# Optimization experiments

Hardware: AMD Instinct MI355X
Metric: run time of the kernel (lower is better)

Reference implementation:

```python
import jax, jax.numpy as jnp
import numpy as np
from jax import lax

BS, CNT, W, P, E, K, L = 32, 128, 2048, 1024, 8, 25, 2


def setup_inputs() -> dict:
    key = jax.random.key(0)
    ks = jax.random.split(key, 12)
    s = lambda k, shape, scale: jax.random.normal(k, shape, dtype=jnp.float32) * scale
    return {
        "x": s(ks[0], (BS, CNT, W), 1.0),
        "conv_w": s(ks[1], (L, E, 1, K), 0.2),
        "conv_b": s(ks[2], (L, E), 0.02),
        "wq": s(ks[3], (L, P, W), 0.02),
        "bq": s(ks[4], (L, P), 0.02),
        "wk": s(ks[5], (L, P, W), 0.02),
        "bk": s(ks[6], (L, P), 0.02),
        "wv": s(ks[7], (L, P, W), 0.02),
        "bv": s(ks[8], (L, P), 0.02),
        "wo": s(ks[9], (L, W, P), 0.02),
        "bo": s(ks[10], (L, W), 0.02),
    }


def _moe(x, w, b):
    # x: [bs, cnt, W]; w: [E, 1, K]; b: [E]
    bs, cnt, d = x.shape
    xf = x.reshape(bs * cnt, 1, d)
    pad = K // 2
    y = lax.conv_general_dilated(
        xf, w, window_strides=(1,), padding=[(pad, pad)],
        dimension_numbers=("NCH", "OIH", "NCH"))  # [bs*cnt, E, W]
    y = y + b[None, :, None]
    return y.mean(axis=1).reshape(bs, cnt, d)


def _fe(x, wq, bq, wk, bk, wv, bv, wo, bo):
    # x: [bs, cnt, W]; projections to P, FFT-domain attention, back to W
    q = jnp.einsum("bcw,pw->bcp", x, wq) + bq
    k = jnp.einsum("bcw,pw->bcp", x, wk) + bk
    v = jnp.einsum("bcw,pw->bcp", x, wv) + bv
    q_fft = jnp.fft.fft(q, axis=-1)
    k_fft = jnp.fft.fft(k, axis=-1)
    v_fft = jnp.fft.fft(v, axis=-1)
    scale = jnp.sqrt(jnp.float32(P))
    weighted = (k_fft * jnp.conj(q_fft)) / scale * v_fft
    wv_real = jnp.fft.ifft(weighted, axis=-1).real.astype(x.dtype)
    return jnp.einsum("bcp,wp->bcw", wv_real, wo) + bo


def reference(x, conv_w, conv_b, wq, bq, wk, bk, wv, bv, wo, bo):
    for l in range(L):
        x = _moe(x, conv_w[l], conv_b[l])
        x = _fe(x, wq[l], bq[l], wk[l], bk[l], wv[l], bv[l], wo[l], bo[l])
    return x
```

## Files before the change

### kernel.cpp

```cpp
#include <hip/hip_runtime.h>
#include <hip/hip_bf16.h>

#define BSZ 32
#define CNTS 128
#define WD 2048
#define PD 1024
#define ED 8
#define KSZ 25
#define LN 2
#define MROWS (BSZ*CNTS)
#define QKVN (3*PD)
#define NWL (PD*WD)

typedef _Float16 f16;
typedef __attribute__((ext_vector_type(8))) _Float16 f16x8;
typedef __attribute__((ext_vector_type(4))) float f32x4;
typedef __attribute__((ext_vector_type(2))) float f32x2;

#define PI_F 3.14159265358979323846f
#define PAD(a) ((a) + ((a) >> 5))

__global__ __launch_bounds__(256) void cvt_layer(
    const float* __restrict__ wq, const float* __restrict__ wk,
    const float* __restrict__ wv, const float* __restrict__ wo,
    f16* __restrict__ wqkv16, f16* __restrict__ wo16)
{
    const int i = (blockIdx.x * 256 + threadIdx.x) * 4;
    const float* src;
    f16* dst;
    if (i < 3*NWL) {
        dst = wqkv16 + i;
        src = (i < NWL) ? wq + i : (i < 2*NWL) ? wk + (i - NWL) : wv + (i - 2*NWL);
    } else {
        dst = wo16 + (i - 3*NWL);
        src = wo + (i - 3*NWL);
    }
    const float4 v = *(const float4*)src;
    f16 o[4];
    o[0] = (f16)v.x; o[1] = (f16)v.y; o[2] = (f16)v.z; o[3] = (f16)v.w;
    *(ushort4*)dst = *(const ushort4*)o;
}

template<typename IT>
__global__ __launch_bounds__(256) void conv_moe(
    const IT* __restrict__ xin,
    const float* __restrict__ cw,
    const float* __restrict__ cb,
    f16* __restrict__ xo)
{
    __shared__ float srow[WD];
    __shared__ float swb[KSZ];
    __shared__ float sbb;
    const int tid = threadIdx.x;
    const size_t row = blockIdx.x;
    if (tid < KSZ) {
        float s = 0.f;
        for (int e = 0; e < ED; ++e) s += cw[e*KSZ + tid];
        swb[tid] = s * (1.f/ED);
    }
    if (tid == 32) {
        float s = 0.f;
        for (int e = 0; e < ED; ++e) s += cb[e];
        sbb = s * (1.f/ED);
    }
    const IT* xr = xin + row*WD;
    for (int i = tid; i < WD; i += 256) srow[i] = (float)xr[i];
    __syncthreads();
    const float bb = sbb;
    for (int t0 = 0; t0 < WD; t0 += 256) {
        const int t = t0 + tid;
        float acc = bb;
        #pragma unroll
        for (int k = 0; k < KSZ; ++k) {
            const int idx = t + k - (KSZ/2);
            const float xv = (idx >= 0 && idx < WD) ? srow[idx] : 0.f;
            acc = fmaf(xv, swb[k], acc);
        }
        xo[row*WD + t] = (f16)acc;
    }
}

template<typename OT>
__global__ __launch_bounds__(256, 2) void gemm_f16(
    const f16* __restrict__ A,
    const f16* __restrict__ B,
    const float* __restrict__ c0, const float* __restrict__ c1, const float* __restrict__ c2,
    OT* __restrict__ out,
    const int K, const int N)
{
    __shared__ f16 sA[128*64];
    __shared__ f16 sB[128*64];
    const int tid  = threadIdx.x;
    const int m0   = blockIdx.x * 128;
    const int n0   = blockIdx.y * 128;
    const int lane = tid & 63;
    const int wave = tid >> 6;
    const int wm   = (wave >> 1) * 64;
    const int wn   = (wave & 1) * 64;
    const int quad = lane >> 4;
    const int r16  = lane & 15;

    f32x4 acc[4][4] = {};

    int arow[4], aoff[4];
    #pragma unroll
    for (int t = 0; t < 4; ++t) {
        const int s = tid + 256*t;
        const int row = s >> 3;
        const int sc8 = ((s & 7) ^ (row & 7)) * 8;
        arow[t] = row;
        aoff[t] = row * K + sc8;
    }

    int aBase[4], aXor[4], bBase[4], bXor[4];
    #pragma unroll
    for (int i = 0; i < 4; ++i) {
        const int ra = wm + i*16 + r16;
        aBase[i] = ra << 3; aXor[i] = ra & 7;
        const int rb = wn + i*16 + r16;
        bBase[i] = rb << 3; bXor[i] = rb & 7;
    }

    const size_t mK = (size_t)m0 * K;
    const size_t nK = (size_t)n0 * K;

    for (int kb = 0; kb < K; kb += 64) {
        #pragma unroll
        for (int t = 0; t < 4; ++t) {
            const int s = tid + 256*t;
            __builtin_amdgcn_global_load_lds(
                (const __attribute__((address_space(1))) unsigned int*)(A + mK + aoff[t] + kb),
                (__attribute__((address_space(3))) unsigned int*)&sA[s*8], 16, 0, 0);
            __builtin_amdgcn_global_load_lds(
                (const __attribute__((address_space(1))) unsigned int*)(B + nK + aoff[t] + kb),
                (__attribute__((address_space(3))) unsigned int*)&sB[s*8], 16, 0, 0);
        }
        __syncthreads();

        #pragma unroll
        for (int ks = 0; ks < 2; ++ks) {
            const int c = ks*4 + quad;
            f16x8 af[4], bfm[4];
            #pragma unroll
            for (int i = 0; i < 4; ++i)
                af[i] = *(const f16x8*)&sA[(aBase[i] | (c ^ aXor[i])) * 8];
            #pragma unroll
            for (int j = 0; j < 4; ++j)
                bfm[j] = *(const f16x8*)&sB[(bBase[j] | (c ^ bXor[j])) * 8];
            #pragma unroll
            for (int i = 0; i < 4; ++i)
                #pragma unroll
                for (int j = 0; j < 4; ++j)
                    acc[i][j] = __builtin_amdgcn_mfma_f32_16x16x32_f16(af[i], bfm[j], acc[i][j], 0, 0, 0);
        }
        __syncthreads();
    }

    #pragma unroll
    for (int j = 0; j < 4; ++j) {
        const int col = n0 + wn + j*16 + r16;
        const float bv = (col < 1024) ? c0[col] : (col < 2048) ? c1[col-1024] : c2[col-2048];
        #pragma unroll
        for (int i = 0; i < 4; ++i) {
            #pragma unroll
            for (int r = 0; r < 4; ++r) {
                const int rowg = m0 + wm + i*16 + quad*4 + r;
                out[(size_t)rowg*N + col] = (OT)(acc[i][j][r] + bv);
            }
        }
    }
}

__global__ __launch_bounds__(512, 2) void gemm256(
    const f16* __restrict__ A,
    const f16* __restrict__ B,
    const float* __restrict__ c0, const float* __restrict__ c1, const float* __restrict__ c2,
    f16* __restrict__ out,
    const int K, const int N)
{
    __shared__ __align__(16) f16 sA[2][2][128*64];
    __shared__ __align__(16) f16 sB[2][2][128*64];

    const int tid  = threadIdx.x;
    const int lane = tid & 63;
    const int wave = tid >> 6;
    const int wr   = wave >> 2;
    const int wc   = wave & 3;
    const int quad = lane >> 4;
    const int r16  = lane & 15;
    const int xr   = r16 & 7;
    const int bHalf = wc >> 1;
    const int bRowB = (wc & 1) * 64;

    const int nwg  = gridDim.x;
    const int orig = blockIdx.x;
    const int wgid = (orig & 7) * (nwg >> 3) + (orig >> 3);
    const int m0   = (wgid & 15) * 256;
    const int n0   = (wgid >> 4) * 256;

    f32x4 acc[8][4] = {};
    f16x8 bf[4][2];

    int soff[2];
    #pragma unroll
    for (int t = 0; t < 2; ++t) {
        const int s = tid + 512*t;
        const int row = s >> 3;
        soff[t] = row * K + (((s & 7) ^ (row & 7)) * 8);
    }

    const f16* Abase[2] = { A + (size_t)m0 * K, A + (size_t)(m0 + 128) * K };
    const f16* Bbase[2] = { B + (size_t)n0 * K, B + (size_t)(n0 + 128) * K };

    #define STAGE(DST, BUF, HALF, GBASE)                                          \
      { _Pragma("unroll") for (int t = 0; t < 2; ++t) {                           \
          __builtin_amdgcn_global_load_lds(                                       \
            (const __attribute__((address_space(1))) unsigned int*)((GBASE) + soff[t]), \
            (__attribute__((address_space(3))) unsigned int*)&DST[BUF][HALF][(tid + 512*t)*8], \
            16, 0, 0); } }

    #define LDFRAG(MAT, BUF, HALF, ROW, C) \
      (*(const f16x8*)&MAT[BUF][HALF][ (((ROW)*8) + ((C) ^ xr)) * 8 ])

    #define WAIT_NONE
    #define WAIT_P4  if (!klast) { asm volatile("s_waitcnt vmcnt(4)" ::: "memory"); } \
                     else        { asm volatile("s_waitcnt vmcnt(0)" ::: "memory"); }
    #define WAIT_P8  if (!klast) { asm volatile("s_waitcnt vmcnt(4)" ::: "memory"); }

    #define PHASE(BUF, Q, WAIT, ...)                                              \
    {                                                                             \
      if ((Q) == 0) {                                                             \
        _Pragma("unroll") for (int j = 0; j < 4; ++j) {                           \
          bf[j][0] = LDFRAG(sB, BUF, bHalf, bRowB + j*16 + r16, quad);            \
          bf[j][1] = LDFRAG(sB, BUF, bHalf, bRowB + j*16 + r16, 4 + quad);        \
        }                                                                         \
      }                                                                           \
      f16x8 a00 = LDFRAG(sA, BUF, wr, (2*(Q))*16   + r16, quad);                  \
      f16x8 a01 = LDFRAG(sA, BUF, wr, (2*(Q))*16   + r16, 4 + quad);              \
      f16x8 a10 = LDFRAG(sA, BUF, wr, (2*(Q)+1)*16 + r16, quad);                  \
      f16x8 a11 = LDFRAG(sA, BUF, wr, (2*(Q)+1)*16 + r16, 4 + quad);              \
      __VA_ARGS__;                                                                \
      __builtin_amdgcn_s_barrier();                                               \
      asm volatile("s_waitcnt lgkmcnt(0)" ::: "memory");                          \
      __builtin_amdgcn_sched_barrier(0);                                          \
      __builtin_amdgcn_s_setprio(1);                                              \
      _Pragma("unroll") for (int j = 0; j < 4; ++j) {                             \
        acc[2*(Q)][j]   = __builtin_amdgcn_mfma_f32_16x16x32_f16(a00, bf[j][0], acc[2*(Q)][j],   0,0,0); \
        acc[2*(Q)+1][j] = __builtin_amdgcn_mfma_f32_16x16x32_f16(a10, bf[j][0], acc[2*(Q)+1][j], 0,0,0); \
      }                                                                           \
      _Pragma("unroll") for (int j = 0; j < 4; ++j) {                             \
        acc[2*(Q)][j]   = __builtin_amdgcn_mfma_f32_16x16x32_f16(a01, bf[j][1], acc[2*(Q)][j],   0,0,0); \
        acc[2*(Q)+1][j] = __builtin_amdgcn_mfma_f32_16x16x32_f16(a11, bf[j][1], acc[2*(Q)+1][j], 0,0,0); \
      }                                                                           \
      __builtin_amdgcn_s_setprio(0);                                              \
      WAIT;                                                                       \
      __builtin_amdgcn_s_barrier();                                               \
    }

    STAGE(sB, 0, 0, Bbase[0]);
    STAGE(sB, 0, 1, Bbase[1]);
    STAGE(sA, 0, 0, Abase[0]);
    STAGE(sA, 0, 1, Abase[1]);
    STAGE(sB, 1, 0, Bbase[0] + 64);
    STAGE(sB, 1, 1, Bbase[1] + 64);
    asm volatile("s_waitcnt vmcnt(4)" ::: "memory");
    __builtin_amdgcn_s_barrier();

    const int NIT = K >> 7;
    for (int it = 0; it < NIT; ++it) {
        const bool klast = (it == NIT - 1);
        const int kb1 = (2*it + 1) * 64;
        const int kb2 = kb1 + 64;
        const int kb3 = kb1 + 128;
        PHASE(0, 0, WAIT_NONE, STAGE(sA, 1, 0, Abase[0] + kb1))
        PHASE(0, 1, WAIT_NONE, STAGE(sA, 1, 1, Abase[1] + kb1))
        PHASE(0, 2, WAIT_NONE, if (!klast) STAGE(sB, 0, 0, Bbase[0] + kb2))
        PHASE(0, 3, WAIT_P4,   if (!klast) STAGE(sB, 0, 1, Bbase[1] + kb2))
        PHASE(1, 0, WAIT_NONE, if (!klast) STAGE(sA, 0, 0, Abase[0] + kb2))
        PHASE(1, 1, WAIT_NONE, if (!klast) STAGE(sA, 0, 1, Abase[1] + kb2))
        PHASE(1, 2, WAIT_NONE, if (!klast) STAGE(sB, 1, 0, Bbase[0] + kb3))
        PHASE(1, 3, WAIT_P8,   if (!klast) STAGE(sB, 1, 1, Bbase[1] + kb3))
    }

    #pragma unroll
    for (int j = 0; j < 4; ++j) {
        const int col = n0 + wc*64 + j*16 + r16;
        const float bv = (col < 1024) ? c0[col] : (col < 2048) ? c1[col-1024] : c2[col-2048];
        #pragma unroll
        for (int mi = 0; mi < 8; ++mi) {
            #pragma unroll
            for (int r = 0; r < 4; ++r) {
                const int rowg = m0 + wr*128 + mi*16 + quad*4 + r;
                out[(size_t)rowg*N + col] = (f16)(acc[mi][j][r] + bv);
            }
        }
    }

    #undef STAGE
    #undef LDFRAG
    #undef WAIT_NONE
    #undef WAIT_P4
    #undef WAIT_P8
    #undef PHASE
}

__device__ inline void fft1024r4(f32x2* x, f32x2* y, const int tid)
{
    f32x2* src = x;
    f32x2* dst = y;
    #pragma unroll
    for (int st = 0; st < 5; ++st) {
        const int ls = 2*st;
        const int s  = 1 << ls;
        const int p  = tid >> ls;
        const int q  = tid & (s - 1);
        const float invn = 1.f / (float)(1024 >> ls);
        const f32x2 a = src[PAD(tid)];
        const f32x2 b = src[PAD(tid + 256)];
        const f32x2 c = src[PAD(tid + 512)];
        const f32x2 d = src[PAD(tid + 768)];
        float ws, wc;
        __sincosf(-2.f*PI_F * (float)p * invn, &ws, &wc);
        const float apcx = a.x + c.x, apcy = a.y + c.y;
        const float amcx = a.x - c.x, amcy = a.y - c.y;
        const float bpdx = b.x + d.x, bpdy = b.y + d.y;
        const float bmdx = b.x - d.x, bmdy = b.y - d.y;
        f32x2 y0; y0.x = apcx + bpdx; y0.y = apcy + bpdy;
        const float t1x = amcx + bmdy, t1y = amcy - bmdx;
        const float t2x = apcx - bpdx, t2y = apcy - bpdy;
        const float t3x = amcx - bmdy, t3y = amcy + bmdx;
        const float w2x = wc*wc - ws*ws, w2y = 2.f*wc*ws;
        const float w3x = w2x*wc - w2y*ws, w3y = w2x*ws + w2y*wc;
        f32x2 y1; y1.x = wc*t1x - ws*t1y;   y1.y = wc*t1y + ws*t1x;
        f32x2 y2; y2.x = w2x*t2x - w2y*t2y; y2.y = w2x*t2y + w2y*t2x;
        f32x2 y3; y3.x = w3x*t3x - w3y*t3y; y3.y = w3x*t3y + w3y*t3x;
        const int base = q + ((p * s) << 2);
        dst[PAD(base)]       = y0;
        dst[PAD(base + s)]   = y1;
        dst[PAD(base + 2*s)] = y2;
        dst[PAD(base + 3*s)] = y3;
        __syncthreads();
        f32x2* t = src; src = dst; dst = t;
    }
}

__global__ __launch_bounds__(256) void fft_attn2(
    const f16* __restrict__ qkv, f16* __restrict__ outg)
{
    __shared__ f32x2 X[PAD(1023)+1], Y[PAD(1023)+1];
    const int tid = threadIdx.x;
    const size_t row0 = (size_t)blockIdx.x * 2;
    const f16* r1 = qkv + row0*QKVN;
    const f16* r2 = r1 + QKVN;

    f32x2 V1[4], V2[4], S1[4], S2[4];

    #pragma unroll
    for (int k = 0; k < 4; ++k) {
        const int i = tid + 256*k;
        f32x2 t; t.x = (float)r1[2048+i]; t.y = (float)r2[2048+i];
        X[PAD(i)] = t;
    }
    __syncthreads();
    fft1024r4(X, Y, tid);
    #pragma unroll
    for (int k = 0; k < 4; ++k) {
        const int f = tid + 256*k;
        const int g = (PD - f) & (PD-1);
        const f32x2 z1 = Y[PAD(f)], z2 = Y[PAD(g)];
        V1[k].x = 0.5f*(z1.x + z2.x); V1[k].y = 0.5f*(z1.y - z2.y);
        V2[k].x = 0.5f*(z1.y + z2.y); V2[k].y = 0.5f*(z2.x - z1.x);
    }

    #pragma unroll
    for (int k = 0; k < 4; ++k) {
        const int i = tid + 256*k;
        f32x2 t; t.x = (float)r1[i]; t.y = (float)r1[1024+i];
        X[PAD(i)] = t;
    }
    __syncthreads();
    fft1024r4(X, Y, tid);
    #pragma unroll
    for (int k = 0; k < 4; ++k) {
        const int f = tid + 256*k;
        const int g = (PD - f) & (PD-1);
        const f32x2 z1 = Y[PAD(f)], z2 = Y[PAD(g)];
        const float Qr = 0.5f*(z1.x + z2.x), Qi = 0.5f*(z1.y - z2.y);
        const float Kr = 0.5f*(z1.y + z2.y), Ki = 0.5f*(z2.x - z1.x);
        const float Pr = (Kr*Qr + Ki*Qi) * (1.f/32.f);
        const float Pi = (Ki*Qr - Kr*Qi) * (1.f/32.f);
        S1[k].x = Pr*V1[k].x - Pi*V1[k].y;
        S1[k].y = -(Pr*V1[k].y + Pi*V1[k].x);
    }

    #pragma unroll
    for (int k = 0; k < 4; ++k) {
        const int i = tid + 256*k;
        f32x2 t; t.x = (float)r2[i]; t.y = (float)r2[1024+i];
        X[PAD(i)] = t;
    }
    __syncthreads();
    fft1024r4(X, Y, tid);
    #pragma unroll
    for (int k = 0; k < 4; ++k) {
        const int f = tid + 256*k;
        const int g = (PD - f) & (PD-1);
        const f32x2 z1 = Y[PAD(f)], z2 = Y[PAD(g)];
        const float Qr = 0.5f*(z1.x + z2.x), Qi = 0.5f*(z1.y - z2.y);
        const float Kr = 0.5f*(z1.y + z2.y), Ki = 0.5f*(z2.x - z1.x);
        const float Pr = (Kr*Qr + Ki*Qi) * (1.f/32.f);
        const float Pi = (Ki*Qr - Kr*Qi) * (1.f/32.f);
        S2[k].x = Pr*V2[k].x - Pi*V2[k].y;
        S2[k].y = -(Pr*V2[k].y + Pi*V2[k].x);
    }

    #pragma unroll
    for (int k = 0; k < 4; ++k) {
        const int f = tid + 256*k;
        f32x2 t; t.x = S1[k].x - S2[k].y; t.y = S1[k].y + S2[k].x;
        X[PAD(f)] = t;
    }
    __syncthreads();
    fft1024r4(X, Y, tid);
    f16* o1 = outg + row0*PD;
    f16* o2 = o1 + PD;
    #pragma unroll
    for (int k = 0; k < 4; ++k) {
        const int n = tid + 256*k;
        const f32x2 z = Y[PAD(n)];
        o1[n] = (f16)(z.x * (1.f/1024.f));
        o2[n] = (f16)(z.y * (1.f/1024.f));
    }
}

extern "C" void kernel_launch(void* const* d_in, const int* in_sizes, int n_in,
                              void* d_out, int out_size, void* d_ws, size_t ws_size,
                              hipStream_t stream)
{
    const float* x      = (const float*)d_in[0];
    const float* conv_w = (const float*)d_in[1];
    const float* conv_b = (const float*)d_in[2];
    const float* wq     = (const float*)d_in[3];
    const float* bq     = (const float*)d_in[4];
    const float* wk     = (const float*)d_in[5];
    const float* bk     = (const float*)d_in[6];
    const float* wv     = (const float*)d_in[7];
    const float* bv     = (const float*)d_in[8];
    const float* wo     = (const float*)d_in[9];
    const float* bo     = (const float*)d_in[10];

    char* ws = (char*)d_ws;
    const size_t MB = 1024*1024;
    f16*   wqkv16 = (f16*)(ws);
    f16*   wo16   = (f16*)(ws + 12*MB);
    f16*   qkvbuf = (f16*)(ws + 16*MB);
    f16*   xc16   = (f16*)(ws + 40*MB);
    f16*   xmid   = (f16*)(ws + 56*MB);
    f16*   wvr16  = xc16;

    for (int l = 0; l < LN; ++l) {
        cvt_layer<<<dim3(4*NWL/4/256), dim3(256), 0, stream>>>(
            wq + (size_t)l*NWL, wk + (size_t)l*NWL, wv + (size_t)l*NWL, wo + (size_t)l*NWL,
            wqkv16, wo16);

        if (l == 0)
            conv_moe<float><<<dim3(MROWS), dim3(256), 0, stream>>>(
                x, conv_w, conv_b, xc16);
        else
            conv_moe<f16><<<dim3(MROWS), dim3(256), 0, stream>>>(
                xmid, conv_w + (size_t)l*ED*KSZ, conv_b + (size_t)l*ED, xc16);

        gemm256<<<dim3((MROWS/256)*(QKVN/256)), dim3(512), 0, stream>>>(
            xc16, wqkv16,
            bq + (size_t)l*PD, bk + (size_t)l*PD, bv + (size_t)l*PD,
            qkvbuf, WD, QKVN);

        fft_attn2<<<dim3(MROWS/2), dim3(256), 0, stream>>>(qkvbuf, wvr16);

        if (l == LN-1)
            gemm_f16<float><<<dim3(MROWS/128, WD/128), dim3(256), 0, stream>>>(
                wvr16, wo16,
                bo + (size_t)l*WD, bo + (size_t)l*WD + PD, bo + (size_t)l*WD + PD,
                (float*)d_out, PD, WD);
        else
            gemm_f16<f16><<<dim3(MROWS/128, WD/128), dim3(256), 0, stream>>>(
                wvr16, wo16,
                bo + (size_t)l*WD, bo + (size_t)l*WD + PD, bo + (size_t)l*WD + PD,
                xmid, PD, WD);
    }
}
```

Baseline: 418.5 us.

## Software-pipeline LDS fragment reads and drop per-phase barriers in QKV GEMM

Restructures the 256x256 QKV GEMM main loop. A-fragment LDS reads now run one quarter-step ahead, using partial lgkmcnt waits, and the barrier count drops from two per phase to two per half-iteration. The goal is to overlap LDS latency with MFMA work and cut synchronisation stalls. Workgroup-to-tile mapping also changes to an explicit XCD-aware layout, for better L2 locality of shared A/B tiles. In exchange it uses more fragment registers and depends on fewer barriers to keep the shared buffers race-free.

```diff
diff --git a/kernel.cpp b/kernel.cpp
--- a/kernel.cpp
+++ b/kernel.cpp
@@ -102,13 +102,12 @@
 
     f32x4 acc[4][4] = {};
 
-    int arow[4], aoff[4];
+    int aoff[4];
     #pragma unroll
     for (int t = 0; t < 4; ++t) {
         const int s = tid + 256*t;
         const int row = s >> 3;
         const int sc8 = ((s & 7) ^ (row & 7)) * 8;
-        arow[t] = row;
         aoff[t] = row * K + sc8;
     }
 
@@ -192,14 +191,17 @@
     const int bHalf = wc >> 1;
     const int bRowB = (wc & 1) * 64;
 
-    const int nwg  = gridDim.x;
     const int orig = blockIdx.x;
-    const int wgid = (orig & 7) * (nwg >> 3) + (orig >> 3);
-    const int m0   = (wgid & 15) * 256;
-    const int n0   = (wgid >> 4) * 256;
+    const int xcd  = orig & 7;
+    const int loc  = orig >> 3;
+    const int mt   = (xcd >> 1) * 4 + (loc & 3);
+    const int nt   = (xcd & 1) * 6 + (loc >> 2);
+    const int m0   = mt * 256;
+    const int n0   = nt * 256;
 
     f32x4 acc[8][4] = {};
     f16x8 bf[4][2];
+    f16x8 aX0, aX1, aX2, aX3, aY0, aY1, aY2, aY3, aZ0, aZ1, aZ2, aZ3;
 
     int soff[2];
     #pragma unroll
@@ -222,40 +224,34 @@
     #define LDFRAG(MAT, BUF, HALF, ROW, C) \
       (*(const f16x8*)&MAT[BUF][HALF][ (((ROW)*8) + ((C) ^ xr)) * 8 ])
 
-    #define WAIT_NONE
-    #define WAIT_P4  if (!klast) { asm volatile("s_waitcnt vmcnt(4)" ::: "memory"); } \
-                     else        { asm volatile("s_waitcnt vmcnt(0)" ::: "memory"); }
-    #define WAIT_P8  if (!klast) { asm volatile("s_waitcnt vmcnt(4)" ::: "memory"); }
-
-    #define PHASE(BUF, Q, WAIT, ...)                                              \
-    {                                                                             \
-      if ((Q) == 0) {                                                             \
-        _Pragma("unroll") for (int j = 0; j < 4; ++j) {                           \
+    #define READ_BF(BUF)                                                          \
+      { _Pragma("unroll") for (int j = 0; j < 4; ++j) {                           \
           bf[j][0] = LDFRAG(sB, BUF, bHalf, bRowB + j*16 + r16, quad);            \
           bf[j][1] = LDFRAG(sB, BUF, bHalf, bRowB + j*16 + r16, 4 + quad);        \
-        }                                                                         \
-      }                                                                           \
-      f16x8 a00 = LDFRAG(sA, BUF, wr, (2*(Q))*16   + r16, quad);                  \
-      f16x8 a01 = LDFRAG(sA, BUF, wr, (2*(Q))*16   + r16, 4 + quad);              \
-      f16x8 a10 = LDFRAG(sA, BUF, wr, (2*(Q)+1)*16 + r16, quad);                  \
-      f16x8 a11 = LDFRAG(sA, BUF, wr, (2*(Q)+1)*16 + r16, 4 + quad);              \
-      __VA_ARGS__;                                                                \
-      __builtin_amdgcn_s_barrier();                                               \
-      asm volatile("s_waitcnt lgkmcnt(0)" ::: "memory");                          \
-      __builtin_amdgcn_sched_barrier(0);                                          \
+        } }
+
+    #define READ_A(BUF, Q, D0, D1, D2, D3)                                        \
+      D0 = LDFRAG(sA, BUF, wr, (2*(Q))*16   + r16, quad);                         \
+      D1 = LDFRAG(sA, BUF, wr, (2*(Q))*16   + r16, 4 + quad);                     \
+      D2 = LDFRAG(sA, BUF, wr, (2*(Q)+1)*16 + r16, quad);                         \
+      D3 = LDFRAG(sA, BUF, wr, (2*(Q)+1)*16 + r16, 4 + quad);
+
+    #define MFMA_Q(Q, D0, D1, D2, D3)                                             \
       __builtin_amdgcn_s_setprio(1);                                              \
-      _Pragma("unroll") for (int j = 0; j < 4; ++j) {                             \
-        acc[2*(Q)][j]   = __builtin_amdgcn_mfma_f32_16x16x32_f16(a00, bf[j][0], acc[2*(Q)][j],   0,0,0); \
-        acc[2*(Q)+1][j] = __builtin_amdgcn_mfma_f32_16x16x32_f16(a10, bf[j][0], acc[2*(Q)+1][j], 0,0,0); \
-      }                                                                           \
-      _Pragma("unroll") for (int j = 0; j < 4; ++j) {                             \
-        acc[2*(Q)][j]   = __builtin_amdgcn_mfma_f32_16x16x32_f16(a01, bf[j][1], acc[2*(Q)][j],   0,0,0); \
-        acc[2*(Q)+1][j] = __builtin_amdgcn_mfma_f32_16x16x32_f16(a11, bf[j][1], acc[2*(Q)+1][j], 0,0,0); \
-      }                                                                           \
-      __builtin_amdgcn_s_setprio(0);                                              \
-      WAIT;                                                                       \
-      __builtin_amdgcn_s_barrier();                                               \
-    }
+      { _Pragma("unroll") for (int jj = 0; jj < 4; ++jj) {                        \
+          acc[2*(Q)][jj]   = __builtin_amdgcn_mfma_f32_16x16x32_f16(D0, bf[jj][0], acc[2*(Q)][jj],   0,0,0); \
+          acc[2*(Q)+1][jj] = __builtin_amdgcn_mfma_f32_16x16x32_f16(D2, bf[jj][0], acc[2*(Q)+1][jj], 0,0,0); \
+        } }                                                                       \
+      { _Pragma("unroll") for (int jj = 0; jj < 4; ++jj) {                        \
+          acc[2*(Q)][jj]   = __builtin_amdgcn_mfma_f32_16x16x32_f16(D1, bf[jj][1], acc[2*(Q)][jj],   0,0,0); \
+          acc[2*(Q)+1][jj] = __builtin_amdgcn_mfma_f32_16x16x32_f16(D3, bf[jj][1], acc[2*(Q)+1][jj], 0,0,0); \
+        } }                                                                       \
+      __builtin_amdgcn_s_setprio(0);
+
+    #define LGKM(n) asm volatile("s_waitcnt lgkmcnt(" #n ")" ::: "memory");       \
+                    __builtin_amdgcn_sched_barrier(0);
+    #define VMC(n)  asm volatile("s_waitcnt vmcnt(" #n ")" ::: "memory");
+    #define BAR()   __builtin_amdgcn_s_barrier();
 
     STAGE(sB, 0, 0, Bbase[0]);
     STAGE(sB, 0, 1, Bbase[1]);
@@ -263,23 +259,57 @@
     STAGE(sA, 0, 1, Abase[1]);
     STAGE(sB, 1, 0, Bbase[0] + 64);
     STAGE(sB, 1, 1, Bbase[1] + 64);
-    asm volatile("s_waitcnt vmcnt(4)" ::: "memory");
-    __builtin_amdgcn_s_barrier();
+    VMC(4)
+    BAR()
 
     const int NIT = K >> 7;
     for (int it = 0; it < NIT; ++it) {
-        const bool klast = (it == NIT - 1);
+        const bool kl = (it == NIT - 1);
         const int kb1 = (2*it + 1) * 64;
         const int kb2 = kb1 + 64;
         const int kb3 = kb1 + 128;
-        PHASE(0, 0, WAIT_NONE, STAGE(sA, 1, 0, Abase[0] + kb1))
-        PHASE(0, 1, WAIT_NONE, STAGE(sA, 1, 1, Abase[1] + kb1))
-        PHASE(0, 2, WAIT_NONE, if (!klast) STAGE(sB, 0, 0, Bbase[0] + kb2))
-        PHASE(0, 3, WAIT_P4,   if (!klast) STAGE(sB, 0, 1, Bbase[1] + kb2))
-        PHASE(1, 0, WAIT_NONE, if (!klast) STAGE(sA, 0, 0, Abase[0] + kb2))
-        PHASE(1, 1, WAIT_NONE, if (!klast) STAGE(sA, 0, 1, Abase[1] + kb2))
-        PHASE(1, 2, WAIT_NONE, if (!klast) STAGE(sB, 1, 0, Bbase[0] + kb3))
-        PHASE(1, 3, WAIT_P8,   if (!klast) STAGE(sB, 1, 1, Bbase[1] + kb3))
+
+        STAGE(sA, 1, 0, Abase[0] + kb1);
+        READ_BF(0)
+        READ_A(0, 0, aX0, aX1, aX2, aX3)
+        LGKM(0)
+        MFMA_Q(0, aX0, aX1, aX2, aX3)
+        BAR()
+        STAGE(sA, 1, 1, Abase[1] + kb1);
+        READ_A(0, 1, aY0, aY1, aY2, aY3)
+        READ_A(0, 2, aZ0, aZ1, aZ2, aZ3)
+        LGKM(4)
+        MFMA_Q(1, aY0, aY1, aY2, aY3)
+        if (!kl) STAGE(sB, 0, 0, Bbase[0] + kb2);
+        READ_A(0, 3, aX0, aX1, aX2, aX3)
+        LGKM(4)
+        MFMA_Q(2, aZ0, aZ1, aZ2, aZ3)
+        if (!kl) STAGE(sB, 0, 1, Bbase[1] + kb2);
+        LGKM(0)
+        MFMA_Q(3, aX0, aX1, aX2, aX3)
+        if (!kl) { VMC(4) } else { VMC(0) }
+        BAR()
+
+        if (!kl) STAGE(sA, 0, 0, Abase[0] + kb2);
+        READ_BF(1)
+        READ_A(1, 0, aX0, aX1, aX2, aX3)
+        LGKM(0)
+        MFMA_Q(0, aX0, aX1, aX2, aX3)
+        BAR()
+        if (!kl) STAGE(sA, 0, 1, Abase[1] + kb2);
+        READ_A(1, 1, aY0, aY1, aY2, aY3)
+        READ_A(1, 2, aZ0, aZ1, aZ2, aZ3)
+        LGKM(4)
+        MFMA_Q(1, aY0, aY1, aY2, aY3)
+        if (!kl) STAGE(sB, 1, 0, Bbase[0] + kb3);
+        READ_A(1, 3, aX0, aX1, aX2, aX3)
+        LGKM(4)
+        MFMA_Q(2, aZ0, aZ1, aZ2, aZ3)
+        if (!kl) STAGE(sB, 1, 1, Bbase[1] + kb3);
+        LGKM(0)
+        MFMA_Q(3, aX0, aX1, aX2, aX3)
+        if (!kl) { VMC(4) }
+        BAR()
     }
 
     #pragma unroll
@@ -298,10 +328,12 @@
 
     #undef STAGE
     #undef LDFRAG
-    #undef WAIT_NONE
-    #undef WAIT_P4
-    #undef WAIT_P8
-    #undef PHASE
+    #undef READ_BF
+    #undef READ_A
+    #undef MFMA_Q
+    #undef LGKM
+    #undef VMC
+    #undef BAR
 }
 
 __device__ inline void fft1024r4(f32x2* x, f32x2* y, const int tid)
```

New measurement: 405.1 us. 3.2% less time.
